# Performance work log

Hardware: AMD Instinct MI355X
Metric: run time of the kernel (lower is better)

Reference implementation:

```python
import jax, jax.numpy as jnp
import numpy as np

B, D, H = 4096, 1024, 1024
LN_EPS = 1e-5


def setup_inputs() -> dict:
    key = jax.random.key(0)
    ks = jax.random.split(key, 5)
    return {
        "x": jax.random.normal(ks[0], (B, D), dtype=jnp.float32),
        "prev_h": jax.random.normal(ks[1], (B, H), dtype=jnp.float32),
        "prev_c": jax.random.normal(ks[2], (B, H), dtype=jnp.float32),
        "Wx": jax.random.normal(ks[3], (D, 4 * H), dtype=jnp.float32) * 0.01,
        "Wh": jax.random.normal(ks[4], (H, 4 * H), dtype=jnp.float32) * 0.01,
        "b": jnp.zeros((4 * H,), dtype=jnp.float32),
        "ln_gamma": jnp.ones((4 * H,), dtype=jnp.float32),
        "ln_beta": jnp.zeros((4 * H,), dtype=jnp.float32),
    }


def reference(x, prev_h, prev_c, Wx, Wh, b, ln_gamma, ln_beta):
    # pre-activations: [B, 4H]
    a = x @ Wx + prev_h @ Wh + b
    # LayerNorm over last dim (use_ln=True)
    mu = jnp.mean(a, axis=-1, keepdims=True)
    var = jnp.mean(jnp.square(a - mu), axis=-1, keepdims=True)
    a = (a - mu) * jax.lax.rsqrt(var + LN_EPS) * ln_gamma + ln_beta
    i = jax.nn.sigmoid(a[:, :H])
    f = jax.nn.sigmoid(a[:, H:2 * H])
    o = jax.nn.sigmoid(a[:, 2 * H:3 * H])
    g = jnp.tanh(a[:, 3 * H:])
    next_c = f * prev_c + i * g
    next_h = o * jnp.tanh(next_c)
    # dropout=0.0 -> identity
    return (next_h, next_c)
```

## Files before the change

kernel.cpp:

```cpp
#include <hip/hip_runtime.h>
#include <hip/hip_bf16.h>
#include <stdint.h>

typedef unsigned short u16;
typedef __attribute__((ext_vector_type(8))) short short8;
typedef __attribute__((ext_vector_type(16))) float f32x16;

#define B_DIM 4096
#define D_DIM 1024
#define H_DIM 1024
#define K_DIM 2048
#define N_DIM 4096
#define LN_EPS 1e-5f

__device__ __forceinline__ u16 f2bf(float f) {
    union { float f; uint32_t u; } v; v.f = f;
    uint32_t u = v.u;
    uint32_t r = (u + 0x7FFFu + ((u >> 16) & 1u)) >> 16;
    return (u16)r;
}
__device__ __forceinline__ float bf2f(u16 h) {
    union { uint32_t u; float f; } v; v.u = ((uint32_t)h) << 16;
    return v.f;
}
__device__ __forceinline__ void gld16(const u16* g, u16* l) {
    __builtin_amdgcn_global_load_lds(
        (const __attribute__((address_space(1))) void*)g,
        (__attribute__((address_space(3))) void*)l,
        16, 0, 0);
}
__device__ __forceinline__ float sigm(float x) { return 1.0f / (1.0f + __expf(-x)); }
__device__ __forceinline__ float tanh_fast(float x) { return 1.0f - 2.0f / (__expf(2.0f * x) + 1.0f); }

__global__ __launch_bounds__(256) void prep(const float* __restrict__ x,
                                            const float* __restrict__ h,
                                            const float* __restrict__ Wx,
                                            const float* __restrict__ Wh,
                                            u16* __restrict__ A,
                                            u16* __restrict__ Bt) {
    __shared__ u16 tile[64 * 64];
    const int t = threadIdx.x;
    if (blockIdx.x < 4096) {
        int id = blockIdx.x * 256 + t;
        int row = id >> 8;
        int col = (id & 255) * 8;
        const float* src = (col < D_DIM) ? (x + (size_t)row * D_DIM + col)
                                         : (h + (size_t)row * H_DIM + (col - D_DIM));
        float4 v0 = ((const float4*)src)[0];
        float4 v1 = ((const float4*)src)[1];
        union { u16 us[8]; uint4 u; } p;
        p.us[0] = f2bf(v0.x); p.us[1] = f2bf(v0.y); p.us[2] = f2bf(v0.z); p.us[3] = f2bf(v0.w);
        p.us[4] = f2bf(v1.x); p.us[5] = f2bf(v1.y); p.us[6] = f2bf(v1.z); p.us[7] = f2bf(v1.w);
        *(uint4*)(A + (size_t)id * 8) = p.u;
    } else {
        const int v = blockIdx.x - 4096;
        const int n0 = (v & 63) * 64;
        const int k0 = (v >> 6) * 64;
        const int kl  = t >> 4;
        const int nl4 = (t & 15) * 4;
#pragma unroll
        for (int it = 0; it < 4; ++it) {
            const int klocal = kl + it * 16;
            const int k = k0 + klocal;
            const float* src = (k < D_DIM) ? (Wx + (size_t)k * N_DIM)
                                           : (Wh + (size_t)(k - D_DIM) * N_DIM);
            float4 w = *(const float4*)(src + n0 + nl4);
            union { u16 us[4]; uint2 u; } p;
            p.us[0] = f2bf(w.x); p.us[1] = f2bf(w.y); p.us[2] = f2bf(w.z); p.us[3] = f2bf(w.w);
            const int swz = 8 * ((klocal >> 4) & 3);
            *(uint2*)(tile + klocal * 64 + (nl4 ^ swz)) = p.u;
        }
        __syncthreads();
        const int nl = t >> 2;
        const int kp = (t & 3) * 16;
        const int swz = 8 * (t & 3);
        union { u16 us[16]; uint4 q[2]; } o;
#pragma unroll
        for (int i = 0; i < 16; ++i)
            o.us[i] = tile[(kp + i) * 64 + (nl ^ swz)];
        u16* dst = Bt + (size_t)(n0 + nl) * K_DIM + k0 + kp;
        *(uint4*)dst = o.q[0];
        *(uint4*)(dst + 8) = o.q[1];
    }
}

__global__ __launch_bounds__(512, 2) void gemm_bf16(const u16* __restrict__ A,
                                                    const u16* __restrict__ Bt,
                                                    const float* __restrict__ bias,
                                                    u16* __restrict__ C) {
    __shared__ u16 As[2][2][8192];
    __shared__ u16 Bs[2][2][8192];
    const int tid = threadIdx.x;
    const int wave = tid >> 6, lane = tid & 63;

    const int bid = blockIdx.y * 16 + blockIdx.x;
    const int swz_bid = (bid & 7) * 32 + (bid >> 3);
    const int m0 = (swz_bid >> 4) * 256;
    const int n0 = (swz_bid & 15) * 256;

    const int wr = wave & 1, wc = wave >> 1;
    const int wm = wr * 128, wn = wc * 64;
    const int lr = lane & 31, half = lane >> 5;

    f32x16 acc[4][2] = {};

    const int srow = wave * 16 + (lane >> 2);
    const int qsrc = (lane & 3) ^ ((lane >> 3) & 3);
    const u16* Asrc = A  + (size_t)(m0 + srow) * K_DIM + qsrc * 8;
    const u16* Bsrc = Bt + (size_t)(n0 + srow) * K_DIM + qsrc * 8;
    const int ldst = wave * 512;

    auto stageA = [&](int buf, int tt, int ks) {
        const int ko = tt * 64 + ks * 32;
        gld16(Asrc + ko,                         &As[buf][ks][ldst]);
        gld16(Asrc + ko + (size_t)128 * K_DIM,   &As[buf][ks][ldst + 4096]);
    };
    auto stageB = [&](int buf, int tt, int ks) {
        const int ko = tt * 64 + ks * 32;
        gld16(Bsrc + ko,                         &Bs[buf][ks][ldst]);
        gld16(Bsrc + ko + (size_t)128 * K_DIM,   &Bs[buf][ks][ldst + 4096]);
    };

    const int sA = (lr >> 1) & 3;
    const int aoff = (wm + lr) * 32;
    const int boff = (wn + lr) * 32;

    short8 af[2][4], bf[2];

#define PHASE(BUF, KS, QJ, READ_A, STAGE_STMT, DO_VM)                                  \
    {                                                                                  \
        if (READ_A) {                                                                  \
            _Pragma("unroll")                                                          \
            for (int kk = 0; kk < 2; ++kk)                                             \
                _Pragma("unroll")                                                      \
                for (int i = 0; i < 4; ++i)                                            \
                    af[kk][i] = *(const short8*)(                                      \
                        &As[BUF][KS][aoff + i * 1024 + (((kk * 2 + half) ^ sA) << 3)]);\
        }                                                                              \
        _Pragma("unroll")                                                              \
        for (int kk = 0; kk < 2; ++kk)                                                 \
            bf[kk] = *(const short8*)(                                                 \
                &Bs[BUF][KS][boff + (QJ) * 1024 + (((kk * 2 + half) ^ sA) << 3)]);     \
        STAGE_STMT;                                                                    \
        __builtin_amdgcn_s_setprio(1);                                                 \
        _Pragma("unroll")                                                              \
        for (int kk = 0; kk < 2; ++kk)                                                 \
            _Pragma("unroll")                                                          \
            for (int i = 0; i < 4; ++i)                                                \
                acc[i][QJ] = __builtin_amdgcn_mfma_f32_32x32x16_bf16(                  \
                    af[kk][i], bf[kk], acc[i][QJ], 0, 0, 0);                           \
        __builtin_amdgcn_s_setprio(0);                                                 \
        if (DO_VM) asm volatile("s_waitcnt vmcnt(8)" ::: "memory");                    \
        __builtin_amdgcn_s_barrier();                                                  \
        asm volatile("" ::: "memory");                                                 \
    }

    stageA(0, 0, 0); stageB(0, 0, 0);
    stageA(0, 0, 1); stageB(0, 0, 1);
    stageA(1, 1, 0); stageB(1, 1, 0);
    asm volatile("s_waitcnt vmcnt(0)" ::: "memory");
    __builtin_amdgcn_s_barrier();
    asm volatile("" ::: "memory");

    for (int it = 0; it < 16; ++it) {
        const int t = it * 2;
        PHASE(0, 0, 0, true,  stageA(1, t + 1, 1), false);
        PHASE(0, 0, 1, false, stageB(1, t + 1, 1), true );
        PHASE(0, 1, 1, true,  stageA(0, t + 2, 0), false);
        PHASE(0, 1, 0, false, stageB(0, t + 2, 0), true );
        PHASE(1, 0, 0, true,  stageA(0, t + 2, 1), false);
        PHASE(1, 0, 1, false, stageB(0, t + 2, 1), true );
        PHASE(1, 1, 1, true,  stageA(1, t + 3, 0), false);
        PHASE(1, 1, 0, false, stageB(1, t + 3, 0), true );
    }
#undef PHASE

#pragma unroll
    for (int i = 0; i < 4; ++i) {
#pragma unroll
        for (int j = 0; j < 2; ++j) {
            const int c = n0 + wn + 32 * j + lr;
            const float bb = bias[c];
#pragma unroll
            for (int reg = 0; reg < 16; ++reg) {
                const int row = m0 + wm + 32 * i + (reg & 3) + 8 * (reg >> 2) + 4 * half;
                C[(size_t)row * N_DIM + c] = f2bf(acc[i][j][reg] + bb);
            }
        }
    }
}

__global__ __launch_bounds__(256) void ln_lstm(const u16* __restrict__ aT,
                                               const float* __restrict__ pc,
                                               const float* __restrict__ gamma,
                                               const float* __restrict__ beta,
                                               float* __restrict__ out) {
    const int row = blockIdx.x;
    const int t = threadIdx.x;
    const u16* ar = aT + (size_t)row * N_DIM;
    const int j0 = t * 4;

    union U2 { uint2 u; u16 us[4]; };
    U2 g4[4];
#pragma unroll
    for (int s = 0; s < 4; ++s) g4[s].u = *(const uint2*)(ar + s * H_DIM + j0);

    float sum = 0.f, ssq = 0.f;
#pragma unroll
    for (int s = 0; s < 4; ++s)
#pragma unroll
        for (int e = 0; e < 4; ++e) { float v = bf2f(g4[s].us[e]); sum += v; ssq += v * v; }

#pragma unroll
    for (int off = 32; off > 0; off >>= 1) {
        sum += __shfl_down(sum, off, 64);
        ssq += __shfl_down(ssq, off, 64);
    }
    __shared__ float red[8];
    if ((t & 63) == 0) { red[t >> 6] = sum; red[4 + (t >> 6)] = ssq; }
    __syncthreads();
    const float ts = red[0] + red[1] + red[2] + red[3];
    const float tq = red[4] + red[5] + red[6] + red[7];
    const float mu = ts * (1.0f / N_DIM);
    const float var = fmaxf(tq * (1.0f / N_DIM) - mu * mu, 0.0f);
    const float rs = rsqrtf(var + LN_EPS);

    float vi[4], vf[4], vo[4], vg[4];
    auto gate = [&](int s, float* v) {
        const int off = s * H_DIM;
        float4 gm = *(const float4*)(gamma + off + j0);
        float4 bt = *(const float4*)(beta + off + j0);
        v[0] = (bf2f(g4[s].us[0]) - mu) * rs * gm.x + bt.x;
        v[1] = (bf2f(g4[s].us[1]) - mu) * rs * gm.y + bt.y;
        v[2] = (bf2f(g4[s].us[2]) - mu) * rs * gm.z + bt.z;
        v[3] = (bf2f(g4[s].us[3]) - mu) * rs * gm.w + bt.w;
    };
    gate(0, vi); gate(1, vf); gate(2, vo); gate(3, vg);

    float4 c4 = *(const float4*)(pc + (size_t)row * H_DIM + j0);
    float cin[4] = {c4.x, c4.y, c4.z, c4.w};
    float nh[4], nc[4];
#pragma unroll
    for (int r = 0; r < 4; ++r) {
        float ig = sigm(vi[r]);
        float fg = sigm(vf[r]);
        float og = sigm(vo[r]);
        float gg = tanh_fast(vg[r]);
        nc[r] = fg * cin[r] + ig * gg;
        nh[r] = og * tanh_fast(nc[r]);
    }
    float4 h4 = {nh[0], nh[1], nh[2], nh[3]};
    float4 c4o = {nc[0], nc[1], nc[2], nc[3]};
    *(float4*)(out + (size_t)row * H_DIM + j0) = h4;
    *(float4*)(out + (size_t)B_DIM * H_DIM + (size_t)row * H_DIM + j0) = c4o;
}

extern "C" void kernel_launch(void* const* d_in, const int* in_sizes, int n_in,
                              void* d_out, int out_size, void* d_ws, size_t ws_size,
                              hipStream_t stream) {
    const float* x  = (const float*)d_in[0];
    const float* ph = (const float*)d_in[1];
    const float* pc = (const float*)d_in[2];
    const float* Wx = (const float*)d_in[3];
    const float* Wh = (const float*)d_in[4];
    const float* b  = (const float*)d_in[5];
    const float* gm = (const float*)d_in[6];
    const float* bt = (const float*)d_in[7];
    float* out = (float*)d_out;

    char* ws = (char*)d_ws;
    u16* Abf = (u16*)ws;
    u16* Btb = (u16*)(ws + (size_t)16 * 1024 * 1024);
    u16* aT  = (u16*)(ws + (size_t)32 * 1024 * 1024);

    prep<<<dim3(4096 + 2048), dim3(256), 0, stream>>>(x, ph, Wx, Wh, Abf, Btb);
    gemm_bf16<<<dim3(16, 16), dim3(512), 0, stream>>>(Abf, Btb, b, aT);
    ln_lstm<<<dim3(4096), dim3(256), 0, stream>>>(aT, pc, gm, bt, out);
}
```

Measured before the change: 214.8 us.

## Restructure GEMM mainloop into a four-slot ring with register-prefetched B fragments

Replaces the double-buffered, half-split A/B staging with a four-slot shared-memory ring. Each region loads one combined A+B k-chunk, waits with vmcnt(4) and does all eight MFMAs for that chunk. B fragments for the next slot are read into alternating register sets before the current chunk's MFMAs, hiding LDS latency behind the matrix ops. The intent is a deeper prefetch distance and fewer waitcnt stalls, at the cost of more registers and a second barrier per region.

Result: slower. 221.6 us (+3.2%).

```diff
diff --git a/kernel.cpp b/kernel.cpp
--- a/kernel.cpp
+++ b/kernel.cpp
@@ -88,8 +88,8 @@
                                                     const u16* __restrict__ Bt,
                                                     const float* __restrict__ bias,
                                                     u16* __restrict__ C) {
-    __shared__ u16 As[2][2][8192];
-    __shared__ u16 Bs[2][2][8192];
+    __shared__ u16 As[4][8192];
+    __shared__ u16 Bs[4][8192];
     const int tid = threadIdx.x;
     const int wave = tid >> 6, lane = tid & 63;
 
@@ -98,11 +98,9 @@
     const int m0 = (swz_bid >> 4) * 256;
     const int n0 = (swz_bid & 15) * 256;
 
-    const int wr = wave & 1, wc = wave >> 1;
-    const int wm = wr * 128, wn = wc * 64;
+    const int wm = (wave & 1) * 128;
+    const int wn = (wave >> 1) * 64;
     const int lr = lane & 31, half = lane >> 5;
-
-    f32x16 acc[4][2] = {};
 
     const int srow = wave * 16 + (lane >> 2);
     const int qsrc = (lane & 3) ^ ((lane >> 3) & 3);
@@ -110,70 +108,72 @@
     const u16* Bsrc = Bt + (size_t)(n0 + srow) * K_DIM + qsrc * 8;
     const int ldst = wave * 512;
 
-    auto stageA = [&](int buf, int tt, int ks) {
+    auto stage_slot = [&](int slot, int rho) {
+        const int tt = (rho >> 1) & 31;
+        const int ks = rho & 1;
         const int ko = tt * 64 + ks * 32;
-        gld16(Asrc + ko,                         &As[buf][ks][ldst]);
-        gld16(Asrc + ko + (size_t)128 * K_DIM,   &As[buf][ks][ldst + 4096]);
-    };
-    auto stageB = [&](int buf, int tt, int ks) {
-        const int ko = tt * 64 + ks * 32;
-        gld16(Bsrc + ko,                         &Bs[buf][ks][ldst]);
-        gld16(Bsrc + ko + (size_t)128 * K_DIM,   &Bs[buf][ks][ldst + 4096]);
+        gld16(Asrc + ko,                       &As[slot][ldst]);
+        gld16(Asrc + ko + (size_t)128 * K_DIM, &As[slot][ldst + 4096]);
+        gld16(Bsrc + ko,                       &Bs[slot][ldst]);
+        gld16(Bsrc + ko + (size_t)128 * K_DIM, &Bs[slot][ldst + 4096]);
     };
 
     const int sA = (lr >> 1) & 3;
     const int aoff = (wm + lr) * 32;
     const int boff = (wn + lr) * 32;
 
-    short8 af[2][4], bf[2];
-
-#define PHASE(BUF, KS, QJ, READ_A, STAGE_STMT, DO_VM)                                  \
-    {                                                                                  \
-        if (READ_A) {                                                                  \
-            _Pragma("unroll")                                                          \
-            for (int kk = 0; kk < 2; ++kk)                                             \
-                _Pragma("unroll")                                                      \
-                for (int i = 0; i < 4; ++i)                                            \
-                    af[kk][i] = *(const short8*)(                                      \
-                        &As[BUF][KS][aoff + i * 1024 + (((kk * 2 + half) ^ sA) << 3)]);\
-        }                                                                              \
-        _Pragma("unroll")                                                              \
-        for (int kk = 0; kk < 2; ++kk)                                                 \
-            bf[kk] = *(const short8*)(                                                 \
-                &Bs[BUF][KS][boff + (QJ) * 1024 + (((kk * 2 + half) ^ sA) << 3)]);     \
-        STAGE_STMT;                                                                    \
-        __builtin_amdgcn_s_setprio(1);                                                 \
-        _Pragma("unroll")                                                              \
-        for (int kk = 0; kk < 2; ++kk)                                                 \
-            _Pragma("unroll")                                                          \
-            for (int i = 0; i < 4; ++i)                                                \
-                acc[i][QJ] = __builtin_amdgcn_mfma_f32_32x32x16_bf16(                  \
-                    af[kk][i], bf[kk], acc[i][QJ], 0, 0, 0);                           \
-        __builtin_amdgcn_s_setprio(0);                                                 \
-        if (DO_VM) asm volatile("s_waitcnt vmcnt(8)" ::: "memory");                    \
-        __builtin_amdgcn_s_barrier();                                                  \
-        asm volatile("" ::: "memory");                                                 \
-    }
-
-    stageA(0, 0, 0); stageB(0, 0, 0);
-    stageA(0, 0, 1); stageB(0, 0, 1);
-    stageA(1, 1, 0); stageB(1, 1, 0);
+    f32x16 acc[4][2] = {};
+    short8 af[2][4], bfA[2][2], bfB[2][2];
+
+#define RD_B(DST, SLOT)                                                           \
+    _Pragma("unroll")                                                             \
+    for (int kk = 0; kk < 2; ++kk)                                                \
+        _Pragma("unroll")                                                         \
+        for (int qj = 0; qj < 2; ++qj)                                            \
+            DST[kk][qj] = *(const short8*)(                                       \
+                &Bs[SLOT][boff + qj * 1024 + (((kk * 2 + half) ^ sA) << 3)]);
+
+#define REGION(SLOT, BFC, BFN, NSLOT, RHO)                                        \
+    {                                                                             \
+        RD_B(BFN, NSLOT);                                                         \
+        stage_slot((RHO) & 3, RHO);                                               \
+        asm volatile("s_waitcnt vmcnt(4)" ::: "memory");                          \
+        __builtin_amdgcn_s_barrier();                                             \
+        _Pragma("unroll")                                                         \
+        for (int kk = 0; kk < 2; ++kk)                                            \
+            _Pragma("unroll")                                                     \
+            for (int i = 0; i < 4; ++i)                                           \
+                af[kk][i] = *(const short8*)(                                     \
+                    &As[SLOT][aoff + i * 1024 + (((kk * 2 + half) ^ sA) << 3)]);  \
+        __builtin_amdgcn_s_setprio(1);                                            \
+        _Pragma("unroll")                                                         \
+        for (int kk = 0; kk < 2; ++kk)                                            \
+            _Pragma("unroll")                                                     \
+            for (int i = 0; i < 4; ++i)                                           \
+                _Pragma("unroll")                                                 \
+                for (int qj = 0; qj < 2; ++qj)                                    \
+                    acc[i][qj] = __builtin_amdgcn_mfma_f32_32x32x16_bf16(         \
+                        af[kk][i], BFC[kk][qj], acc[i][qj], 0, 0, 0);             \
+        __builtin_amdgcn_s_setprio(0);                                            \
+        __builtin_amdgcn_s_barrier();                                             \
+        asm volatile("" ::: "memory");                                            \
+    }
+
+    stage_slot(0, 0); stage_slot(1, 1); stage_slot(2, 2);
     asm volatile("s_waitcnt vmcnt(0)" ::: "memory");
     __builtin_amdgcn_s_barrier();
     asm volatile("" ::: "memory");
+    RD_B(bfA, 0);
 
     for (int it = 0; it < 16; ++it) {
-        const int t = it * 2;
-        PHASE(0, 0, 0, true,  stageA(1, t + 1, 1), false);
-        PHASE(0, 0, 1, false, stageB(1, t + 1, 1), true );
-        PHASE(0, 1, 1, true,  stageA(0, t + 2, 0), false);
-        PHASE(0, 1, 0, false, stageB(0, t + 2, 0), true );
-        PHASE(1, 0, 0, true,  stageA(0, t + 2, 1), false);
-        PHASE(1, 0, 1, false, stageB(0, t + 2, 1), true );
-        PHASE(1, 1, 1, true,  stageA(1, t + 3, 0), false);
-        PHASE(1, 1, 0, false, stageB(1, t + 3, 0), true );
-    }
-#undef PHASE
+        const int q0 = it * 4;
+        REGION(0, bfA, bfB, 1, q0 + 3);
+        REGION(1, bfB, bfA, 2, q0 + 4);
+        REGION(2, bfA, bfB, 3, q0 + 5);
+        REGION(3, bfB, bfA, 0, q0 + 6);
+    }
+#undef REGION
+#undef RD_B
 
 #pragma unroll
     for (int i = 0; i < 4; ++i) {
```
